# Kernel tuning notes

Hardware: AMD Instinct MI355X
Metric: run time of the kernel (lower is better)

## Reference

```python
import jax, jax.numpy as jnp
import numpy as np

B, C, N, D = 8192, 1000, 2, 512
EPS = 0.1  # epsilon init arg


def setup_inputs() -> dict:
    key = jax.random.key(0)
    kx, kc, kr = jax.random.split(key, 3)
    x = jax.random.normal(kx, (B, D), dtype=jnp.float32)
    centroids = jax.random.uniform(kc, (C, N, D), minval=-1.0, maxval=1.0, dtype=jnp.float32)
    rej_raw = jax.random.uniform(kr, (C * N, D), minval=-1.0, maxval=1.0, dtype=jnp.float32)
    # replicate the __init__ rescaling of the (frozen) rejective centroids
    cmax = jnp.max(jnp.linalg.norm(centroids, axis=-1))
    rej = 2.0 * cmax * rej_raw / (jnp.linalg.norm(rej_raw, axis=-1, keepdims=True) + 1e-16)
    return {"x": x, "centroids": centroids, "rejective_centroids": rej, "return_dists": 1}


def reference(x, centroids, rejective_centroids, return_dists):
    b, d = x.shape
    c, n, _ = centroids.shape
    t = c * n
    # centroid_norm is updated via .data in torch -> detached
    cnorm = jax.lax.stop_gradient(jnp.max(jnp.linalg.norm(centroids, axis=-1)))
    cf = (centroids / (cnorm + 1e-16)).reshape(t, d)  # [T, D] normalized centroids
    # pairwise L2 distances via the expansion identity (no [B,T,D] intermediate)
    x2 = jnp.sum(x * x, axis=-1)          # [B]
    c2 = jnp.sum(cf * cf, axis=-1)        # [T]
    d2 = jnp.maximum(x2[:, None] + c2[None, :] - 2.0 * (x @ cf.T), 0.0)
    dist = jnp.sqrt(d2)                   # [B, T]
    min_dist_class = jnp.min(dist.reshape(b, c, n), axis=2)  # [B, C]
    y = -min_dist_class
    if return_dists:
        idx = jnp.argmin(dist, axis=1)                 # [B]
        closest = cf[idx]                              # [B, D] gathered closest centroid
        r = rejective_centroids                        # [T, D]
        r2 = jnp.sum(r * r, axis=-1)                   # [T]
        xr = x @ r.T                                   # [B, T]
        cr = closest @ r.T                             # [B, T]
        cx = jnp.sum(closest * x, axis=-1)             # [B]
        cl2 = jnp.sum(closest * closest, axis=-1)      # [B]
        # w = closest - r ; b_off = -w . (closest + r)/2 = -0.5(|c|^2 - |r|^2)
        num = jnp.abs(cx[:, None] - xr - 0.5 * (cl2[:, None] - r2[None, :]))
        den = jnp.sqrt(jnp.maximum(cl2[:, None] + r2[None, :] - 2.0 * cr, 0.0)) + 1e-9
        rej_hd = jnp.min(num / den, axis=-1)           # [B]
        return jnp.concatenate([y, rej_hd[:, None]], axis=1)
    min_d = jnp.min(min_dist_class, axis=1)
    removed = jnp.where(min_dist_class == min_d[:, None], jnp.inf, min_dist_class)
    second = jnp.min(removed, axis=1)
    y_bot = -(1.0 - EPS) / (1.0 + EPS) * second
    accept = min_d - EPS * (min_d + second)
    soft = jax.nn.sigmoid(accept)  # ac_temp == 1
    return jnp.concatenate([y, y_bot[:, None], soft[:, None]], axis=1)
```

## Files before the change

kernel.cpp:

```cpp
#include <hip/hip_runtime.h>
#include <math.h>
#include <stdint.h>

#define NB   8192
#define NCLS 1000
#define NT   2000
#define ND   512
#define OUTW 1001

#define OFF_NORM2C 0
#define OFF_R2     2048
#define OFF_X2     4096
#define OFF_SCAL   12288
#define OFF_IDX    12352
#define OFF_CX     20544
#define OFF_CL2    28736

#define NOFF_MIND  36928
#define NOFF_REJP  823360

#define OFF8_MIND  36928
#define OFF8_MINT  102464
#define OFF8_MDOT  168000
#define OFF8_REJP  233536

#define PACKX_B  (8ull<<20)
#define PACKC_B  (24ull<<20)
#define PACKR_B  (28ull<<20)
#define PACKT_B  (32ull<<20)
#define WS_NEED  (48ull<<20)

typedef __attribute__((ext_vector_type(8))) short bf16x8;
typedef __attribute__((ext_vector_type(4))) float f32x4;

__global__ __launch_bounds__(64) void rownorm_kernel(
    const float* __restrict__ cen, const float* __restrict__ rej,
    const float* __restrict__ x, float* __restrict__ ws)
{
    int row = blockIdx.x;
    int lane = threadIdx.x;
    const float* src;
    int dstoff;
    if (row < NT)        { src = cen + (size_t)row * ND;          dstoff = OFF_NORM2C + row; }
    else if (row < 2*NT) { src = rej + (size_t)(row - NT) * ND;   dstoff = OFF_R2 + (row - NT); }
    else                 { src = x   + (size_t)(row - 2*NT) * ND; dstoff = OFF_X2 + (row - 2*NT); }
    float s = 0.f;
#pragma unroll
    for (int k = 0; k < ND / 64; ++k) { float v = src[lane + k * 64]; s += v * v; }
#pragma unroll
    for (int off = 32; off > 0; off >>= 1) s += __shfl_down(s, off);
    if (lane == 0) ws[dstoff] = s;
}

__global__ __launch_bounds__(256) void maxnorm_kernel(float* __restrict__ ws)
{
    __shared__ float sm[256];
    int tid = threadIdx.x;
    float m = 0.f;
    for (int i = tid; i < NT; i += 256) m = fmaxf(m, ws[OFF_NORM2C + i]);
    sm[tid] = m;
    __syncthreads();
    for (int s = 128; s > 0; s >>= 1) {
        if (tid < s) sm[tid] = fmaxf(sm[tid], sm[tid + s]);
        __syncthreads();
    }
    if (tid == 0) {
        float cnorm = sqrtf(sm[0]);
        float inv = 1.f / (cnorm + 1e-16f);
        ws[OFF_SCAL + 0] = cnorm;
        ws[OFF_SCAL + 1] = inv;
        ws[OFF_SCAL + 2] = inv * inv;
    }
}

__device__ __forceinline__ ushort bf16rn(float f){
    uint32_t u = __float_as_uint(f);
    return (ushort)((u + 0x7fffu + ((u >> 16) & 1u)) >> 16);
}

__global__ __launch_bounds__(256) void pack_kernel(const float* __restrict__ src,
    unsigned char* __restrict__ dst, int validRows)
{
    int tid = threadIdx.x;
    int lane = tid & 63;
    int W = blockIdx.x * 4 + (tid >> 6);
    int s  = W >> 4;
    int ks = W & 15;
    int row = s * 16 + (lane & 15);
    int k   = ks * 32 + (lane >> 4) * 8;
    float v[8];
    if (row < validRows) {
        float4 a = *(const float4*)&src[(size_t)row * ND + k];
        float4 b = *(const float4*)&src[(size_t)row * ND + k + 4];
        v[0]=a.x; v[1]=a.y; v[2]=a.z; v[3]=a.w;
        v[4]=b.x; v[5]=b.y; v[6]=b.z; v[7]=b.w;
    } else {
#pragma unroll
        for (int j = 0; j < 8; ++j) v[j] = 0.f;
    }
    union { ushort h[8]; uint4 q; } H, L;
#pragma unroll
    for (int j = 0; j < 8; ++j) {
        ushort hb = bf16rn(v[j]);
        float hf = __uint_as_float(((uint32_t)hb) << 16);
        H.h[j] = hb;
        L.h[j] = bf16rn(v[j] - hf);
    }
    size_t base = ((size_t)(((s >> 3) * 16 + ks) * 16 + (s & 7) * 2)) * 1024;
    *(uint4*)(dst + base + lane * 16)        = H.q;
    *(uint4*)(dst + base + 1024 + lane * 16) = L.q;
}

typedef __attribute__((address_space(3))) unsigned int lds_u32;
typedef const __attribute__((address_space(1))) unsigned int glb_u32;
__device__ __forceinline__ void gload_lds16(const unsigned char* g, unsigned char* l) {
    __builtin_amdgcn_global_load_lds((glb_u32*)g, (lds_u32*)l, 16, 0, 0);
}

#define SCHED_FENCE __builtin_amdgcn_sched_barrier(0)

#define PASS4(av, bv) do { _Pragma("unroll") \
    for (int qi = 0; qi < 4; ++qi) \
        _Pragma("unroll") \
        for (int ri = 0; ri < 4; ++ri) \
            acc[ri][qi] = __builtin_amdgcn_mfma_f32_16x16x32_bf16( \
                av[ri], bv[qi], acc[ri][qi], 0, 0, 0); \
    } while (0)

__device__ __forceinline__ void stage_dist(
    const unsigned char* __restrict__ aP2, const unsigned char* __restrict__ bP2,
    int ks, unsigned char* lbuf, int wave, int lane)
{
    if (wave < 8) {
#pragma unroll
        for (int j = 0; j < 4; ++j) {
            int gc = wave * 4 + j, s = gc >> 1, pl = gc & 1;
            gload_lds16(aP2 + ((s >> 3) * 16 + ks) * 16384 + ((s & 7) * 2 + pl) * 1024 + lane * 16,
                        lbuf + gc * 1024);
        }
    } else {
#pragma unroll
        for (int j = 0; j < 4; ++j) {
            int gc = (wave - 8) * 4 + j, s = gc >> 1, pl = gc & 1;
            gload_lds16(bP2 + ((s >> 3) * 16 + ks) * 16384 + ((s & 7) * 2 + pl) * 1024 + lane * 16,
                        lbuf + 32768 + gc * 1024);
        }
    }
}

__device__ __forceinline__ void compute_dist(
    const unsigned char* __restrict__ cbuf, int lane, int wr, int wc, f32x4 acc[4][4])
{
    const unsigned char* aB = cbuf + wr * 8192 + lane * 16;
    const unsigned char* bB = cbuf + 32768 + wc * 8192 + lane * 16;
    bf16x8 ah[4], bh[4];
#pragma unroll
    for (int i = 0; i < 4; ++i) {
        ah[i] = *(const bf16x8*)(aB + i * 2048);
        bh[i] = *(const bf16x8*)(bB + i * 2048);
    }
    PASS4(ah, bh);
    {
        bf16x8 bl[4];
#pragma unroll
        for (int i = 0; i < 4; ++i) bl[i] = *(const bf16x8*)(bB + i * 2048 + 1024);
        PASS4(ah, bl);
    }
    {
        bf16x8 al[4];
#pragma unroll
        for (int i = 0; i < 4; ++i) al[i] = *(const bf16x8*)(aB + i * 2048 + 1024);
        PASS4(al, bh);
    }
}

__device__ __forceinline__ void mfma_core_dist(
    const unsigned char* __restrict__ aP2, const unsigned char* __restrict__ bP2,
    unsigned char* lds, int lane, int wave, int wr, int wc, f32x4 acc[4][4])
{
    stage_dist(aP2, bP2, 0, lds, wave, lane);
    for (int ks = 0; ks < 16; ++ks) {
        unsigned char* cbuf = lds + (ks & 1) * 65536;
        unsigned char* nbuf = lds + ((ks + 1) & 1) * 65536;
        if (ks < 15) {
            stage_dist(aP2, bP2, ks + 1, nbuf, wave, lane);
            SCHED_FENCE;
            asm volatile("s_waitcnt vmcnt(4)" ::: "memory");
            SCHED_FENCE;
        } else {
            SCHED_FENCE;
            asm volatile("s_waitcnt vmcnt(0)" ::: "memory");
            SCHED_FENCE;
        }
        __builtin_amdgcn_s_barrier();
        __builtin_amdgcn_s_setprio(1);
        compute_dist(cbuf, lane, wr, wc, acc);
        __builtin_amdgcn_s_setprio(0);
        __builtin_amdgcn_s_barrier();
    }
}

__device__ __forceinline__ void stage_xr(
    const unsigned char* __restrict__ aP2, const unsigned char* __restrict__ bP2,
    int ks2, unsigned char* lbuf, int wave, int lane)
{
#pragma unroll
    for (int j = 0; j < 4; ++j) {
        int q = (wave & 7) * 4 + j;
        int sub = q >> 4, cs = q & 15;
        int ks = ks2 * 2 + sub;
        const unsigned char* src = (wave < 8)
            ? aP2 + ((cs >> 3) * 16 + ks) * 16384 + ((cs & 7) * 2) * 1024 + lane * 16
            : bP2 + ((cs >> 3) * 16 + ks) * 16384 + ((cs & 7) * 2) * 1024 + lane * 16;
        unsigned char* dst = lbuf + (wave < 8 ? 0 : 32768) + sub * 16384 + cs * 1024;
        gload_lds16(src, dst);
    }
}

__device__ __forceinline__ void compute_xr(
    const unsigned char* __restrict__ cbuf, int lane, int wr, int wc, f32x4 acc[4][4])
{
#pragma unroll
    for (int sub = 0; sub < 2; ++sub) {
        const unsigned char* aB = cbuf + sub * 16384 + wr * 4096 + lane * 16;
        const unsigned char* bB = cbuf + 32768 + sub * 16384 + wc * 4096 + lane * 16;
        bf16x8 ah[4], bh[4];
#pragma unroll
        for (int i = 0; i < 4; ++i) {
            ah[i] = *(const bf16x8*)(aB + i * 1024);
            bh[i] = *(const bf16x8*)(bB + i * 1024);
        }
        __builtin_amdgcn_s_setprio(1);
        PASS4(ah, bh);
        __builtin_amdgcn_s_setprio(0);
    }
}

__device__ __forceinline__ void mfma_core_xr(
    const unsigned char* __restrict__ aP2, const unsigned char* __restrict__ bP2,
    unsigned char* lds, int lane, int wave, int wr, int wc, f32x4 acc[4][4])
{
    stage_xr(aP2, bP2, 0, lds, wave, lane);
    for (int ks2 = 0; ks2 < 8; ++ks2) {
        unsigned char* cbuf = lds + (ks2 & 1) * 65536;
        unsigned char* nbuf = lds + ((ks2 + 1) & 1) * 65536;
        if (ks2 < 7) {
            stage_xr(aP2, bP2, ks2 + 1, nbuf, wave, lane);
            SCHED_FENCE;
            asm volatile("s_waitcnt vmcnt(4)" ::: "memory");
            SCHED_FENCE;
        } else {
            SCHED_FENCE;
            asm volatile("s_waitcnt vmcnt(0)" ::: "memory");
            SCHED_FENCE;
        }
        __builtin_amdgcn_s_barrier();
        compute_xr(cbuf, lane, wr, wc, acc);
        __builtin_amdgcn_s_barrier();
    }
}

__global__ __launch_bounds__(1024) void dist_mfma_kernel(
    const unsigned char* __restrict__ xpack, const unsigned char* __restrict__ cpack,
    float* __restrict__ out, float* __restrict__ ws)
{
    __shared__ unsigned char lds[2 * 65536];
    int tid = threadIdx.x, lane = tid & 63, wave = tid >> 6;
    int wr = wave >> 2, wc = wave & 3;
    int xb = blockIdx.x, yb = blockIdx.y;
    int b0 = xb * 256, t0base = yb * 256;
    f32x4 acc[4][4];
#pragma unroll
    for (int i = 0; i < 4; ++i)
#pragma unroll
        for (int q = 0; q < 4; ++q) acc[i][q] = (f32x4){0.f, 0.f, 0.f, 0.f};
    mfma_core_dist(xpack + (size_t)xb * 524288, cpack + (size_t)yb * 524288,
                   lds, lane, wave, wr, wc, acc);

    float inv  = ws[OFF_SCAL + 1];
    float inv2 = ws[OFF_SCAL + 2];
    int rq = lane >> 4, cidx = lane & 15;
    int seg = yb * 4 + wc;
    float c2q[4]; int tq[4];
#pragma unroll
    for (int qi = 0; qi < 4; ++qi) {
        int t = t0base + wc * 64 + qi * 16 + cidx;
        tq[qi] = t;
        c2q[qi] = (t < NT) ? ws[OFF_NORM2C + t] * inv2 : 0.f;
    }
    unsigned long long* keys = (unsigned long long*)(ws + NOFF_MIND);

#pragma unroll
    for (int ri = 0; ri < 4; ++ri) {
#pragma unroll
        for (int reg = 0; reg < 4; ++reg) {
            int row = b0 + wr * 64 + ri * 16 + rq * 4 + reg;
            float x2 = ws[OFF_X2 + row];
            unsigned long long best = ~0ull;
#pragma unroll
            for (int qi = 0; qi < 4; ++qi) {
                float d2 = fmaxf(x2 + c2q[qi] - 2.f * (acc[ri][qi][reg] * inv), 0.f);
                float d2n = __shfl_xor(d2, 1);
                int t = tq[qi];
                if ((t < NT) && ((cidx & 1) == 0))
                    out[(size_t)row * OUTW + (t >> 1)] = -sqrtf(fminf(d2, d2n));
                if (t < NT) {
                    unsigned long long key =
                        ((unsigned long long)__float_as_uint(d2) << 32) | (unsigned)t;
                    best = best < key ? best : key;
                }
            }
#pragma unroll
            for (int off = 1; off < 16; off <<= 1) {
                unsigned long long o = __shfl_xor(best, off);
                best = best < o ? best : o;
            }
            if (cidx == 0) keys[(size_t)row * 32 + seg] = best;
        }
    }
}

__global__ __launch_bounds__(256) void combine32_kernel(float* __restrict__ ws)
{
    int b = blockIdx.x * 256 + threadIdx.x;
    const unsigned long long* keys = (const unsigned long long*)(ws + NOFF_MIND);
    unsigned long long best = keys[(size_t)b * 32];
#pragma unroll
    for (int s = 1; s < 32; ++s) {
        unsigned long long k = keys[(size_t)b * 32 + s];
        best = best < k ? best : k;
    }
    int bt = (int)(best & 0xffffffffull);
    float d2 = __uint_as_float((unsigned)(best >> 32));
    float c2 = ws[OFF_NORM2C + bt] * ws[OFF_SCAL + 2];
    float x2 = ws[OFF_X2 + b];
    ((int*)ws)[OFF_IDX + b] = bt;
    ws[OFF_CX + b] = 0.5f * (x2 + c2 - d2);
    ws[OFF_CL2 + b] = c2;
}

#define LOADA1(buf, ks_) do { _Pragma("unroll") \
    for (int i = 0; i < 4; ++i) { \
        buf[i] = *(const bf16x8*)(aB + (ks_) * 16384 + i * 2048); \
    } } while (0)
#define LOADB1(buf, ks_) do { _Pragma("unroll") \
    for (int i = 0; i < 4; ++i) { \
        buf[i] = *(const bf16x8*)(bB + (ks_) * 16384 + i * 2048); \
    } } while (0)

__device__ __forceinline__ void mfma_core_db1(
    const unsigned char* __restrict__ aP, const unsigned char* __restrict__ bP,
    int lane, int wr, int wc, f32x4 acc[4][4])
{
    const unsigned char* aB = aP + wr * 8192 + lane * 16;
    const unsigned char* bB = bP + wc * 8192 + lane * 16;
    bf16x8 a0[4], a1[4], b0[4], b1[4];
    LOADA1(a0, 0); LOADB1(b0, 0);
    for (int ks = 0; ks < 16; ks += 2) {
        LOADA1(a1, ks + 1); LOADB1(b1, ks + 1);
        PASS4(a0, b0);
        if (ks + 2 < 16) { LOADA1(a0, ks + 2); LOADB1(b0, ks + 2); }
        PASS4(a1, b1);
    }
}

__global__ __launch_bounds__(256, 2) void table_mfma_kernel(
    const unsigned char* __restrict__ cpack, const unsigned char* __restrict__ rpack,
    ushort* __restrict__ table, const float* __restrict__ ws)
{
    int tid = threadIdx.x, lane = tid & 63, wave = tid >> 6;
    int wr = wave >> 1, wc = wave & 1;
    int c0 = blockIdx.x * 128, t0base = blockIdx.y * 128;
    f32x4 acc[4][4];
#pragma unroll
    for (int i = 0; i < 4; ++i)
#pragma unroll
        for (int q = 0; q < 4; ++q) acc[i][q] = (f32x4){0.f, 0.f, 0.f, 0.f};
    mfma_core_db1(cpack + (size_t)blockIdx.x * 262144, rpack + (size_t)blockIdx.y * 262144,
                  lane, wr, wc, acc);

    float inv  = ws[OFF_SCAL + 1];
    float inv2 = ws[OFF_SCAL + 2];
    int rq = lane >> 4, cidx = lane & 15;
    float r2q[4]; int tq[4];
#pragma unroll
    for (int qi = 0; qi < 4; ++qi) {
        int t = t0base + wc * 64 + qi * 16 + cidx;
        tq[qi] = t;
        r2q[qi] = (t < NT) ? ws[OFF_R2 + t] : 0.f;
    }
#pragma unroll
    for (int ri = 0; ri < 4; ++ri) {
#pragma unroll
        for (int reg = 0; reg < 4; ++reg) {
            int c = c0 + wr * 64 + ri * 16 + rq * 4 + reg;
            if (c < NT) {
                float cl2c = ws[OFF_NORM2C + c] * inv2;
#pragma unroll
                for (int qi = 0; qi < 4; ++qi) {
                    int t = tq[qi];
                    if (t < NT) {
                        float cfr = acc[ri][qi][reg] * inv;
                        float den = sqrtf(fmaxf(cl2c + r2q[qi] - 2.f * cfr, 0.f)) + 1e-9f;
                        table[(size_t)c * 2048 + t] = bf16rn(1.f / den);
                    }
                }
            }
        }
    }
}

__global__ __launch_bounds__(1024) void xr_mfma_kernel(
    const unsigned char* __restrict__ xpack, const unsigned char* __restrict__ rpack,
    const ushort* __restrict__ table, float* __restrict__ ws)
{
    __shared__ unsigned char lds[2 * 65536];
    int tid = threadIdx.x, lane = tid & 63, wave = tid >> 6;
    int wr = wave >> 2, wc = wave & 3;
    int xb = blockIdx.x, yb = blockIdx.y;
    int b0 = xb * 256, t0base = yb * 256;
    f32x4 acc[4][4];
#pragma unroll
    for (int i = 0; i < 4; ++i)
#pragma unroll
        for (int q = 0; q < 4; ++q) acc[i][q] = (f32x4){0.f, 0.f, 0.f, 0.f};
    mfma_core_xr(xpack + (size_t)xb * 524288, rpack + (size_t)yb * 524288,
                 lds, lane, wave, wr, wc, acc);

    int rq = lane >> 4, cidx = lane & 15;
    int seg = yb * 4 + wc;
    float r2q[4]; int tq[4];
#pragma unroll
    for (int qi = 0; qi < 4; ++qi) {
        int t = t0base + wc * 64 + qi * 16 + cidx;
        tq[qi] = t;
        r2q[qi] = (t < NT) ? ws[OFF_R2 + t] : 0.f;
    }
#pragma unroll
    for (int ri = 0; ri < 4; ++ri) {
#pragma unroll
        for (int reg = 0; reg < 4; ++reg) {
            int row = b0 + wr * 64 + ri * 16 + rq * 4 + reg;
            int idx = ((const int*)ws)[OFF_IDX + row];
            float cx  = ws[OFF_CX + row];
            float cl2 = ws[OFF_CL2 + row];
            const ushort* trow = table + (size_t)idx * 2048;
            float tv[4];
#pragma unroll
            for (int qi = 0; qi < 4; ++qi)
                tv[qi] = (tq[qi] < NT)
                    ? __uint_as_float(((uint32_t)trow[tq[qi]]) << 16) : 0.f;
            float mv = INFINITY;
#pragma unroll
            for (int qi = 0; qi < 4; ++qi) {
                if (tq[qi] < NT) {
                    float num = fabsf(cx - acc[ri][qi][reg] - 0.5f * (cl2 - r2q[qi]));
                    mv = fminf(mv, num * tv[qi]);
                }
            }
#pragma unroll
            for (int off = 1; off < 16; off <<= 1) mv = fminf(mv, __shfl_xor(mv, off));
            if (cidx == 0) ws[NOFF_REJP + (size_t)row * 32 + seg] = mv;
        }
    }
}

__global__ __launch_bounds__(256) void rejcombine32_kernel(
    const float* __restrict__ ws, float* __restrict__ out)
{
    int b = blockIdx.x * 256 + threadIdx.x;
    float bd = ws[NOFF_REJP + (size_t)b * 32];
#pragma unroll
    for (int s = 1; s < 32; ++s) bd = fminf(bd, ws[NOFF_REJP + (size_t)b * 32 + s]);
    out[(size_t)b * OUTW + NCLS] = bd;
}

#define BK   32
#define LDST 68

__global__ __launch_bounds__(256) void dist_kernel(
    const float* __restrict__ x, const float* __restrict__ cen,
    float* __restrict__ out, float* __restrict__ ws)
{
    __shared__ float Xs[BK][LDST];
    __shared__ float Cs[BK][LDST];
    __shared__ float red_d[64][17];
    __shared__ int   red_t[64][17];
    __shared__ float red_x[64][17];

    int tid = threadIdx.x;
    int tx = tid & 15, ty = tid >> 4;
    int b0 = blockIdx.x * 64;
    int tseg0 = blockIdx.y * 256;
    int tseg1 = min(tseg0 + 256, NT);

    float inv  = ws[OFF_SCAL + 1];
    float inv2 = ws[OFF_SCAL + 2];
    float x2v[4];
#pragma unroll
    for (int i = 0; i < 4; ++i) x2v[i] = ws[OFF_X2 + b0 + ty * 4 + i];

    int lr = tid >> 2;
    int lc = (tid & 3) * 8;

    float mind[4], mdot[4];
    int mint[4];
#pragma unroll
    for (int i = 0; i < 4; ++i) { mind[i] = INFINITY; mint[i] = 0x7fffffff; mdot[i] = 0.f; }

    for (int t0 = tseg0; t0 < tseg1; t0 += 64) {
        float acc[4][4];
#pragma unroll
        for (int i = 0; i < 4; ++i)
#pragma unroll
            for (int jj = 0; jj < 4; ++jj) acc[i][jj] = 0.f;

        for (int k0 = 0; k0 < ND; k0 += BK) {
            {
                const float4 v0 = *(const float4*)&x[(size_t)(b0 + lr) * ND + k0 + lc];
                const float4 v1 = *(const float4*)&x[(size_t)(b0 + lr) * ND + k0 + lc + 4];
                Xs[lc + 0][lr] = v0.x; Xs[lc + 1][lr] = v0.y; Xs[lc + 2][lr] = v0.z; Xs[lc + 3][lr] = v0.w;
                Xs[lc + 4][lr] = v1.x; Xs[lc + 5][lr] = v1.y; Xs[lc + 6][lr] = v1.z; Xs[lc + 7][lr] = v1.w;
            }
            {
                int tr = t0 + lr;
                float4 v0 = make_float4(0.f, 0.f, 0.f, 0.f), v1 = v0;
                if (tr < NT) {
                    v0 = *(const float4*)&cen[(size_t)tr * ND + k0 + lc];
                    v1 = *(const float4*)&cen[(size_t)tr * ND + k0 + lc + 4];
                }
                Cs[lc + 0][lr] = v0.x; Cs[lc + 1][lr] = v0.y; Cs[lc + 2][lr] = v0.z; Cs[lc + 3][lr] = v0.w;
                Cs[lc + 4][lr] = v1.x; Cs[lc + 5][lr] = v1.y; Cs[lc + 6][lr] = v1.z; Cs[lc + 7][lr] = v1.w;
            }
            __syncthreads();
#pragma unroll
            for (int kk = 0; kk < BK; ++kk) {
                float4 av = *(const float4*)&Xs[kk][ty * 4];
                float4 bv = *(const float4*)&Cs[kk][tx * 4];
                float a[4] = {av.x, av.y, av.z, av.w};
                float bb[4] = {bv.x, bv.y, bv.z, bv.w};
#pragma unroll
                for (int i = 0; i < 4; ++i)
#pragma unroll
                    for (int jj = 0; jj < 4; ++jj)
                        acc[i][jj] = fmaf(a[i], bb[jj], acc[i][jj]);
            }
            __syncthreads();
        }

        float distv[4][4];
#pragma unroll
        for (int jj = 0; jj < 4; ++jj) {
            int t = t0 + tx * 4 + jj;
            bool valid = (t < NT);
            float c2 = valid ? ws[OFF_NORM2C + t] * inv2 : 0.f;
#pragma unroll
            for (int i = 0; i < 4; ++i) {
                float dsc = acc[i][jj] * inv;
                float d2 = x2v[i] + c2 - 2.f * dsc;
                float dd = sqrtf(fmaxf(d2, 0.f));
                distv[i][jj] = dd;
                if (valid && (dd < mind[i])) { mind[i] = dd; mint[i] = t; mdot[i] = dsc; }
            }
        }
#pragma unroll
        for (int jp = 0; jp < 2; ++jp) {
            int t = t0 + tx * 4 + jp * 2;
            if (t < NT) {
                int cls = t >> 1;
#pragma unroll
                for (int i = 0; i < 4; ++i) {
                    out[(size_t)(b0 + ty * 4 + i) * OUTW + cls] =
                        -fminf(distv[i][jp * 2], distv[i][jp * 2 + 1]);
                }
            }
        }
    }

#pragma unroll
    for (int i = 0; i < 4; ++i) {
        red_d[ty * 4 + i][tx] = mind[i];
        red_t[ty * 4 + i][tx] = mint[i];
        red_x[ty * 4 + i][tx] = mdot[i];
    }
    __syncthreads();
    if (tid < 64) {
        float bd = red_d[tid][0]; int bt = red_t[tid][0]; float bx = red_x[tid][0];
        for (int q = 1; q < 16; ++q) {
            float d = red_d[tid][q]; int tt = red_t[tid][q];
            if (d < bd || (d == bd && tt < bt)) { bd = d; bt = tt; bx = red_x[tid][q]; }
        }
        int b = b0 + tid;
        int s = blockIdx.y;
        ws[OFF8_MIND + b * 8 + s] = bd;
        ((int*)ws)[OFF8_MINT + b * 8 + s] = bt;
        ws[OFF8_MDOT + b * 8 + s] = bx;
    }
}

__global__ __launch_bounds__(256) void combine_kernel(float* __restrict__ ws)
{
    int b = blockIdx.x * 256 + threadIdx.x;
    float bd = ws[OFF8_MIND + b * 8];
    int   bt = ((int*)ws)[OFF8_MINT + b * 8];
    float bx = ws[OFF8_MDOT + b * 8];
#pragma unroll
    for (int s = 1; s < 8; ++s) {
        float d = ws[OFF8_MIND + b * 8 + s];
        int  tt = ((int*)ws)[OFF8_MINT + b * 8 + s];
        if (d < bd || (d == bd && tt < bt)) { bd = d; bt = tt; bx = ws[OFF8_MDOT + b * 8 + s]; }
    }
    ((int*)ws)[OFF_IDX + b] = bt;
    ws[OFF_CX + b] = bx;
    ws[OFF_CL2 + b] = ws[OFF_NORM2C + bt] * ws[OFF_SCAL + 2];
}

__global__ __launch_bounds__(256) void rej_kernel(
    const float* __restrict__ x, const float* __restrict__ cen,
    const float* __restrict__ rej, float* __restrict__ ws)
{
    __shared__ float Xs[BK][LDST];
    __shared__ float Rs[BK][LDST];
    __shared__ float Ls[BK][LDST];
    __shared__ int idxL[64];
    __shared__ float red_d[64][17];

    int tid = threadIdx.x;
    int tx = tid & 15, ty = tid >> 4;
    int b0 = blockIdx.x * 64;
    int tseg0 = blockIdx.y * 256;
    int tseg1 = min(tseg0 + 256, NT);
    float inv = ws[OFF_SCAL + 1];

    if (tid < 64) idxL[tid] = ((int*)ws)[OFF_IDX + b0 + tid];
    float cxv[4], cl2v[4];
#pragma unroll
    for (int i = 0; i < 4; ++i) {
        cxv[i]  = ws[OFF_CX  + b0 + ty * 4 + i];
        cl2v[i] = ws[OFF_CL2 + b0 + ty * 4 + i];
    }
    __syncthreads();

    int lr = tid >> 2, lc = (tid & 3) * 8;
    int myrow = idxL[lr];

    float minv[4] = {INFINITY, INFINITY, INFINITY, INFINITY};

    for (int t0 = tseg0; t0 < tseg1; t0 += 64) {
        float xr[4][4], cr[4][4];
#pragma unroll
        for (int i = 0; i < 4; ++i)
#pragma unroll
            for (int jj = 0; jj < 4; ++jj) { xr[i][jj] = 0.f; cr[i][jj] = 0.f; }

        for (int k0 = 0; k0 < ND; k0 += BK) {
            {
                const float4 v0 = *(const float4*)&x[(size_t)(b0 + lr) * ND + k0 + lc];
                const float4 v1 = *(const float4*)&x[(size_t)(b0 + lr) * ND + k0 + lc + 4];
                Xs[lc + 0][lr] = v0.x; Xs[lc + 1][lr] = v0.y; Xs[lc + 2][lr] = v0.z; Xs[lc + 3][lr] = v0.w;
                Xs[lc + 4][lr] = v1.x; Xs[lc + 5][lr] = v1.y; Xs[lc + 6][lr] = v1.z; Xs[lc + 7][lr] = v1.w;
            }
            {
                const float4 v0 = *(const float4*)&cen[(size_t)myrow * ND + k0 + lc];
                const float4 v1 = *(const float4*)&cen[(size_t)myrow * ND + k0 + lc + 4];
                Ls[lc + 0][lr] = v0.x * inv; Ls[lc + 1][lr] = v0.y * inv;
                Ls[lc + 2][lr] = v0.z * inv; Ls[lc + 3][lr] = v0.w * inv;
                Ls[lc + 4][lr] = v1.x * inv; Ls[lc + 5][lr] = v1.y * inv;
                Ls[lc + 6][lr] = v1.z * inv; Ls[lc + 7][lr] = v1.w * inv;
            }
            {
                int tr = t0 + lr;
                float4 v0 = make_float4(0.f, 0.f, 0.f, 0.f), v1 = v0;
                if (tr < NT) {
                    v0 = *(const float4*)&rej[(size_t)tr * ND + k0 + lc];
                    v1 = *(const float4*)&rej[(size_t)tr * ND + k0 + lc + 4];
                }
                Rs[lc + 0][lr] = v0.x; Rs[lc + 1][lr] = v0.y; Rs[lc + 2][lr] = v0.z; Rs[lc + 3][lr] = v0.w;
                Rs[lc + 4][lr] = v1.x; Rs[lc + 5][lr] = v1.y; Rs[lc + 6][lr] = v1.z; Rs[lc + 7][lr] = v1.w;
            }
            __syncthreads();
#pragma unroll
            for (int kk = 0; kk < BK; ++kk) {
                float4 av = *(const float4*)&Xs[kk][ty * 4];
                float4 lv = *(const float4*)&Ls[kk][ty * 4];
                float4 rv = *(const float4*)&Rs[kk][tx * 4];
                float a[4] = {av.x, av.y, av.z, av.w};
                float l[4] = {lv.x, lv.y, lv.z, lv.w};
                float r[4] = {rv.x, rv.y, rv.z, rv.w};
#pragma unroll
                for (int i = 0; i < 4; ++i)
#pragma unroll
                    for (int jj = 0; jj < 4; ++jj) {
                        xr[i][jj] = fmaf(a[i], r[jj], xr[i][jj]);
                        cr[i][jj] = fmaf(l[i], r[jj], cr[i][jj]);
                    }
            }
            __syncthreads();
        }

#pragma unroll
        for (int jj = 0; jj < 4; ++jj) {
            int t = t0 + tx * 4 + jj;
            if (t < NT) {
                float r2 = ws[OFF_R2 + t];
#pragma unroll
                for (int i = 0; i < 4; ++i) {
                    float num = fabsf(cxv[i] - xr[i][jj] - 0.5f * (cl2v[i] - r2));
                    float den = sqrtf(fmaxf(cl2v[i] + r2 - 2.f * cr[i][jj], 0.f)) + 1e-9f;
                    minv[i] = fminf(minv[i], num / den);
                }
            }
        }
    }

#pragma unroll
    for (int i = 0; i < 4; ++i) red_d[ty * 4 + i][tx] = minv[i];
    __syncthreads();
    if (tid < 64) {
        float bd = red_d[tid][0];
        for (int q = 1; q < 16; ++q) bd = fminf(bd, red_d[tid][q]);
        ws[OFF8_REJP + (size_t)(b0 + tid) * 8 + blockIdx.y] = bd;
    }
}

__global__ __launch_bounds__(256) void rejcombine_kernel(
    const float* __restrict__ ws, float* __restrict__ out)
{
    int b = blockIdx.x * 256 + threadIdx.x;
    float bd = ws[OFF8_REJP + b * 8];
#pragma unroll
    for (int s = 1; s < 8; ++s) bd = fminf(bd, ws[OFF8_REJP + b * 8 + s]);
    out[(size_t)b * OUTW + NCLS] = bd;
}

extern "C" void kernel_launch(void* const* d_in, const int* in_sizes, int n_in,
                              void* d_out, int out_size, void* d_ws, size_t ws_size,
                              hipStream_t stream)
{
    const float* x   = (const float*)d_in[0];
    const float* cen = (const float*)d_in[1];
    const float* rej = (const float*)d_in[2];
    float* out = (float*)d_out;
    float* ws  = (float*)d_ws;
    unsigned char* wsb = (unsigned char*)d_ws;

    rownorm_kernel<<<2 * NT + NB, 64, 0, stream>>>(cen, rej, x, ws);
    maxnorm_kernel<<<1, 256, 0, stream>>>(ws);

    if (ws_size >= WS_NEED) {
        pack_kernel<<<2048, 256, 0, stream>>>(x,   wsb + PACKX_B, NB);
        pack_kernel<<<512,  256, 0, stream>>>(cen, wsb + PACKC_B, NT);
        pack_kernel<<<512,  256, 0, stream>>>(rej, wsb + PACKR_B, NT);
        dist_mfma_kernel<<<dim3(32, 8), 1024, 0, stream>>>(wsb + PACKX_B, wsb + PACKC_B, out, ws);
        combine32_kernel<<<32, 256, 0, stream>>>(ws);
        table_mfma_kernel<<<dim3(16, 16), 256, 0, stream>>>(wsb + PACKC_B, wsb + PACKR_B,
                                                            (ushort*)(wsb + PACKT_B), ws);
        xr_mfma_kernel<<<dim3(32, 8), 1024, 0, stream>>>(wsb + PACKX_B, wsb + PACKR_B,
                                                         (const ushort*)(wsb + PACKT_B), ws);
        rejcombine32_kernel<<<32, 256, 0, stream>>>(ws, out);
    } else {
        dist_kernel<<<dim3(NB / 64, 8), 256, 0, stream>>>(x, cen, out, ws);
        combine_kernel<<<NB / 256, 256, 0, stream>>>(ws);
        rej_kernel<<<dim3(NB / 64, 8), 256, 0, stream>>>(x, cen, rej, ws);
        rejcombine_kernel<<<NB / 256, 256, 0, stream>>>(ws, out);
    }
}
```

Baseline: 153.0 us.

## Fuse row squared-norm computation into pack kernels and batch epilogue loads

On the main path, squared row norms for x, centroids and rejective centroids are now accumulated inside the bf16 pack kernels via wave shuffles and atomicAdd, after a memset of the norm region. This drops the separate rownorm pass that reread all three inputs. The dist and xr epilogues also hoist per-row workspace loads and table gathers ahead of the compute loops to expose memory-level parallelism. Atomic float adds make the norm summation order nondeterministic, and an extra memset launch is added.

```diff
diff --git a/kernel.cpp b/kernel.cpp
--- a/kernel.cpp
+++ b/kernel.cpp
@@ -79,7 +79,7 @@
 }
 
 __global__ __launch_bounds__(256) void pack_kernel(const float* __restrict__ src,
-    unsigned char* __restrict__ dst, int validRows)
+    unsigned char* __restrict__ dst, int validRows, float* __restrict__ sums)
 {
     int tid = threadIdx.x;
     int lane = tid & 63;
@@ -98,6 +98,13 @@
 #pragma unroll
         for (int j = 0; j < 8; ++j) v[j] = 0.f;
     }
+    float ss = 0.f;
+#pragma unroll
+    for (int j = 0; j < 8; ++j) ss += v[j] * v[j];
+    ss += __shfl_xor(ss, 16);
+    ss += __shfl_xor(ss, 32);
+    if (lane < 16 && row < validRows) atomicAdd(&sums[row], ss);
+
     union { ushort h[8]; uint4 q; } H, L;
 #pragma unroll
     for (int j = 0; j < 8; ++j) {
@@ -292,14 +299,17 @@
 
 #pragma unroll
     for (int ri = 0; ri < 4; ++ri) {
+        float x2v[4];
+#pragma unroll
+        for (int reg = 0; reg < 4; ++reg)
+            x2v[reg] = ws[OFF_X2 + b0 + wr * 64 + ri * 16 + rq * 4 + reg];
 #pragma unroll
         for (int reg = 0; reg < 4; ++reg) {
             int row = b0 + wr * 64 + ri * 16 + rq * 4 + reg;
-            float x2 = ws[OFF_X2 + row];
             unsigned long long best = ~0ull;
 #pragma unroll
             for (int qi = 0; qi < 4; ++qi) {
-                float d2 = fmaxf(x2 + c2q[qi] - 2.f * (acc[ri][qi][reg] * inv), 0.f);
+                float d2 = fmaxf(x2v[reg] + c2q[qi] - 2.f * (acc[ri][qi][reg] * inv), 0.f);
                 float d2n = __shfl_xor(d2, 1);
                 int t = tq[qi];
                 if ((t < NT) && ((cidx & 1) == 0))
@@ -438,24 +448,32 @@
     }
 #pragma unroll
     for (int ri = 0; ri < 4; ++ri) {
+        int idxv[4]; float cxv[4], cl2v[4];
 #pragma unroll
         for (int reg = 0; reg < 4; ++reg) {
             int row = b0 + wr * 64 + ri * 16 + rq * 4 + reg;
-            int idx = ((const int*)ws)[OFF_IDX + row];
-            float cx  = ws[OFF_CX + row];
-            float cl2 = ws[OFF_CL2 + row];
-            const ushort* trow = table + (size_t)idx * 2048;
-            float tv[4];
+            idxv[reg] = ((const int*)ws)[OFF_IDX + row];
+            cxv[reg]  = ws[OFF_CX + row];
+            cl2v[reg] = ws[OFF_CL2 + row];
+        }
+        float tv[4][4];
+#pragma unroll
+        for (int reg = 0; reg < 4; ++reg) {
+            const ushort* trow = table + (size_t)idxv[reg] * 2048;
 #pragma unroll
             for (int qi = 0; qi < 4; ++qi)
-                tv[qi] = (tq[qi] < NT)
+                tv[reg][qi] = (tq[qi] < NT)
                     ? __uint_as_float(((uint32_t)trow[tq[qi]]) << 16) : 0.f;
+        }
+#pragma unroll
+        for (int reg = 0; reg < 4; ++reg) {
+            int row = b0 + wr * 64 + ri * 16 + rq * 4 + reg;
             float mv = INFINITY;
 #pragma unroll
             for (int qi = 0; qi < 4; ++qi) {
                 if (tq[qi] < NT) {
-                    float num = fabsf(cx - acc[ri][qi][reg] - 0.5f * (cl2 - r2q[qi]));
-                    mv = fminf(mv, num * tv[qi]);
+                    float num = fabsf(cxv[reg] - acc[ri][qi][reg] - 0.5f * (cl2v[reg] - r2q[qi]));
+                    mv = fminf(mv, num * tv[reg][qi]);
                 }
             }
 #pragma unroll
@@ -744,13 +762,12 @@
     float* ws  = (float*)d_ws;
     unsigned char* wsb = (unsigned char*)d_ws;
 
-    rownorm_kernel<<<2 * NT + NB, 64, 0, stream>>>(cen, rej, x, ws);
-    maxnorm_kernel<<<1, 256, 0, stream>>>(ws);
-
     if (ws_size >= WS_NEED) {
-        pack_kernel<<<2048, 256, 0, stream>>>(x,   wsb + PACKX_B, NB);
-        pack_kernel<<<512,  256, 0, stream>>>(cen, wsb + PACKC_B, NT);
-        pack_kernel<<<512,  256, 0, stream>>>(rej, wsb + PACKR_B, NT);
+        hipMemsetAsync(d_ws, 0, 12288 * sizeof(float), stream);
+        pack_kernel<<<2048, 256, 0, stream>>>(x,   wsb + PACKX_B, NB, ws + OFF_X2);
+        pack_kernel<<<512,  256, 0, stream>>>(cen, wsb + PACKC_B, NT, ws + OFF_NORM2C);
+        pack_kernel<<<512,  256, 0, stream>>>(rej, wsb + PACKR_B, NT, ws + OFF_R2);
+        maxnorm_kernel<<<1, 256, 0, stream>>>(ws);
         dist_mfma_kernel<<<dim3(32, 8), 1024, 0, stream>>>(wsb + PACKX_B, wsb + PACKC_B, out, ws);
         combine32_kernel<<<32, 256, 0, stream>>>(ws);
         table_mfma_kernel<<<dim3(16, 16), 256, 0, stream>>>(wsb + PACKC_B, wsb + PACKR_B,
@@ -759,6 +776,8 @@
                                                          (const ushort*)(wsb + PACKT_B), ws);
         rejcombine32_kernel<<<32, 256, 0, stream>>>(ws, out);
     } else {
+        rownorm_kernel<<<2 * NT + NB, 64, 0, stream>>>(cen, rej, x, ws);
+        maxnorm_kernel<<<1, 256, 0, stream>>>(ws);
         dist_kernel<<<dim3(NB / 64, 8), 256, 0, stream>>>(x, cen, out, ws);
         combine_kernel<<<NB / 256, 256, 0, stream>>>(ws);
         rej_kernel<<<dim3(NB / 64, 8), 256, 0, stream>>>(x, cen, rej, ws);
```

Result: no change. 154.4 us (+0.9%).
